# Kernel tuning notes

Measured on AMD Instinct MI355X. Metric: run time of the kernel, lower is better.

Reference implementation:

```python
import jax, jax.numpy as jnp
import numpy as np
import math

# Model config (see init_kwargs)
E = 1024   # emb_size
H = 8      # ffwd_num_head
D = 128    # ffwd_head_size (E == H*D)
NE = 16    # ffwd_num_expert
A = 2      # ffwd_num_expert_active
S = 256    # ffwd_expert_size
B = 2      # batch_size_fwd
T = 2048   # context_window
NUM_BLOCK = 12


def setup_inputs() -> dict:
    key = jax.random.key(0)
    ks = jax.random.split(key, 5)
    x = jax.random.normal(ks[0], (B, T, E), jnp.float32)
    # fc_in_fused: Linear(E, 4E+NE, bias=False), torch weight shape (out,in)
    w_in = 0.02 * jax.random.normal(ks[1], (4 * E + NE, E), jnp.float32)
    # fc_out_fused: Linear(2E, E), std 0.02/sqrt(num_block)
    w_out = (0.02 / math.sqrt(NUM_BLOCK)) * jax.random.normal(ks[2], (E, 2 * E), jnp.float32)
    # k_ffwd/v_ffwd: original (1,H,NE*S,D); stored here as (NE,H,S,D) for per-expert scan
    k_ffwd = 0.02 * jax.random.normal(ks[3], (NE, H, S, D), jnp.float32)
    v_ffwd = 0.02 * jax.random.normal(ks[4], (NE, H, S, D), jnp.float32)
    return {"x": x, "w_in": w_in, "w_out": w_out, "k_ffwd": k_ffwd, "v_ffwd": v_ffwd}


def _rope(t):
    # Standard half-split RoPE, base 10000. t: (B,T,H,D)
    half = t.shape[-1] // 2
    inv_freq = 1.0 / (10000.0 ** (jnp.arange(half, dtype=jnp.float32) / half))
    ang = jnp.arange(t.shape[1], dtype=jnp.float32)[:, None] * inv_freq  # (T, half)
    cos = jnp.cos(ang)[None, :, None, :]
    sin = jnp.sin(ang)[None, :, None, :]
    t1, t2 = t[..., :half], t[..., half:]
    return jnp.concatenate([t1 * cos - t2 * sin, t1 * sin + t2 * cos], axis=-1)


def reference(x, w_in, w_out, k_ffwd, v_ffwd):
    Bx, Tx, _ = x.shape
    h = x @ w_in.T  # (B,T,4E+NE)
    q_f, q_a, k_a, v_a, router_logits = jnp.split(h, [E, 2 * E, 3 * E, 4 * E], axis=-1)

    # top-k routing (order of the k slots is irrelevant: outputs are summed)
    gate_logits, assign = jax.lax.top_k(router_logits, A)  # (B,T,A)
    gate = jax.nn.sigmoid(gate_logits)

    # --- attention half: causal softmax attention, scale 1/sqrt(D), with RoPE ---
    q = _rope(q_a.reshape(Bx, Tx, H, D))
    k = _rope(k_a.reshape(Bx, Tx, H, D))
    v = v_a.reshape(Bx, Tx, H, D)
    scores = jnp.einsum('bqhd,bkhd->bhqk', q, k) / math.sqrt(D)
    causal = jnp.tril(jnp.ones((Tx, Tx), dtype=bool))
    scores = jnp.where(causal, scores, -jnp.inf)
    p = jax.nn.softmax(scores, axis=-1)
    attn_out = jnp.einsum('bhqk,bkhd->bqhd', p, v).reshape(Bx, Tx, E)

    # --- MoE-FFN half, expressed as attention with score_mod log1p(gelu):
    # exp(lse)*softmax recovers sum_s (1+gelu(q.k_s)) v_s; subtracting sum_s v_s
    # leaves sum_s gelu(q.k_s) v_s over the assigned expert's slots. ---
    qf = q_f.reshape(Bx, Tx, H, D)

    def step(acc, ekv):
        e, ke, ve = ekv  # ke, ve: (H,S,D)
        s = jnp.einsum('bthd,hsd->bths', qf, ke)
        a = jax.nn.gelu(s, approximate=False)  # torch F.gelu default = exact erf
        o = jnp.einsum('bths,hsd->bthd', a, ve)
        g = jnp.sum(jnp.where(assign == e, gate, 0.0), axis=-1)  # (B,T)
        return acc + g[..., None, None] * o, None

    acc0 = jnp.zeros((Bx, Tx, H, D), x.dtype)
    ffwd_out, _ = jax.lax.scan(step, acc0, (jnp.arange(NE), k_ffwd, v_ffwd))
    ffwd_out = ffwd_out.reshape(Bx, Tx, E)

    out = jnp.concatenate([attn_out, ffwd_out], axis=-1) @ w_out.T  # (B,T,E)
    return out
```

## Files before the change

kernel.cpp:

```cpp
#include <hip/hip_runtime.h>
#include <hip/hip_bf16.h>
#include <math.h>

#define E 1024
#define NEXP 16
#define HH 8
#define DD 128
#define SS 256
#define BB 2
#define TT 2048
#define BT 4096

typedef __attribute__((ext_vector_type(8))) short bf16x8;
typedef __attribute__((ext_vector_type(4))) float f32x4;

#define GLDS16(g, s) __builtin_amdgcn_global_load_lds( \
    (const __attribute__((address_space(1))) void*)(g), \
    (__attribute__((address_space(3))) void*)(s), 16, 0, 0)

__device__ __forceinline__ ushort f2b(float f) {
    union { float f; unsigned u; } v; v.f = f;
    unsigned r = (v.u + 0x7FFFu + ((v.u >> 16) & 1u)) >> 16;
    return (ushort)r;
}
__device__ __forceinline__ float b2f(ushort u) {
    union { unsigned u; float f; } v; v.u = ((unsigned)u) << 16;
    return v.f;
}
__device__ __forceinline__ float gelu_fast(float x) {
    float u2 = x * x;
    float tu = x * (1.5957691216f + 0.0713548163f * u2);
    float e = __expf(tu);
    float sig = 1.f - __builtin_amdgcn_rcpf(e + 1.f);
    return x * sig;
}

__global__ __launch_bounds__(256) void prep(
    const float* __restrict__ w_in, const float* __restrict__ w_out,
    const float* __restrict__ kf, const float* __restrict__ vf,
    const float* __restrict__ x,
    ushort* __restrict__ wib, ushort* __restrict__ wob,
    ushort* __restrict__ kfb, ushort* __restrict__ vtf,
    float* __restrict__ gval, int* __restrict__ eidx, ushort* __restrict__ xb)
{
    __shared__ float T[64][132];
    const int bx = blockIdx.x;
    const int t = threadIdx.x;

    if (bx >= 3584) {
        const int m = (bx - 3584) * 4 + (t >> 6);
        const int lane = t & 63;

        const float* xp = x + (size_t)m * 1024 + lane * 4;
        float4 xv0 = *(const float4*)(xp);
        float4 xv1 = *(const float4*)(xp + 256);
        float4 xv2 = *(const float4*)(xp + 512);
        float4 xv3 = *(const float4*)(xp + 768);

        {
            const int swrow = (m & 7) << 4;
            char* xrow = (char*)xb + (size_t)m * 2048;
            ushort4 u;
            u.x = f2b(xv0.x); u.y = f2b(xv0.y); u.z = f2b(xv0.z); u.w = f2b(xv0.w);
            *(ushort4*)(xrow + ((lane * 8 + 0 * 512) ^ swrow)) = u;
            u.x = f2b(xv1.x); u.y = f2b(xv1.y); u.z = f2b(xv1.z); u.w = f2b(xv1.w);
            *(ushort4*)(xrow + ((lane * 8 + 1 * 512) ^ swrow)) = u;
            u.x = f2b(xv2.x); u.y = f2b(xv2.y); u.z = f2b(xv2.z); u.w = f2b(xv2.w);
            *(ushort4*)(xrow + ((lane * 8 + 2 * 512) ^ swrow)) = u;
            u.x = f2b(xv3.x); u.y = f2b(xv3.y); u.z = f2b(xv3.z); u.w = f2b(xv3.w);
            *(ushort4*)(xrow + ((lane * 8 + 3 * 512) ^ swrow)) = u;
        }

        float p[16];
        #pragma unroll
        for (int e = 0; e < 16; ++e) {
            const float* wp = w_in + (size_t)(4096 + e) * 1024 + lane * 4;
            float4 w0 = *(const float4*)(wp);
            float4 w1 = *(const float4*)(wp + 256);
            float4 w2 = *(const float4*)(wp + 512);
            float4 w3 = *(const float4*)(wp + 768);
            float s0 = xv0.x * w0.x + xv0.y * w0.y + xv0.z * w0.z + xv0.w * w0.w;
            float s1 = xv1.x * w1.x + xv1.y * w1.y + xv1.z * w1.z + xv1.w * w1.w;
            float s2 = xv2.x * w2.x + xv2.y * w2.y + xv2.z * w2.z + xv2.w * w2.w;
            float s3 = xv3.x * w3.x + xv3.y * w3.y + xv3.z * w3.z + xv3.w * w3.w;
            p[e] = (s0 + s1) + (s2 + s3);
        }
        #pragma unroll
        for (int d = 1; d < 64; d <<= 1) {
            #pragma unroll
            for (int e = 0; e < 16; ++e)
                p[e] += __shfl_xor(p[e], d);
        }
        float best = -1e30f; int bi = 0;
        #pragma unroll
        for (int e = 0; e < 16; ++e)
            if (p[e] > best) { best = p[e]; bi = e; }
        float best2 = -1e30f; int bi2 = 0;
        #pragma unroll
        for (int e = 0; e < 16; ++e)
            if (e != bi && p[e] > best2) { best2 = p[e]; bi2 = e; }

        if (lane == 0) {
            gval[m * 2 + 0] = 1.f / (1.f + __expf(-best));
            gval[m * 2 + 1] = 1.f / (1.f + __expf(-best2));
            eidx[m * 2 + 0] = bi;
            eidx[m * 2 + 1] = bi2;
        }
        return;
    }

    if (bx < 3072) {
        const float* in;
        ushort* outp;
        int kshift, i;
        if (bx < 2048) { in = w_in;  outp = wib; kshift = 10; i = (bx * 256 + t) * 8; }
        else           { in = w_out; outp = wob; kshift = 11; i = ((bx - 2048) * 256 + t) * 8; }
        int row = i >> kshift;
        int colb = (i - (row << kshift)) * 2;
        float4 f0 = *(const float4*)(in + i);
        float4 f1 = *(const float4*)(in + i + 4);
        ushort4 u0, u1;
        u0.x = f2b(f0.x); u0.y = f2b(f0.y); u0.z = f2b(f0.z); u0.w = f2b(f0.w);
        u1.x = f2b(f1.x); u1.y = f2b(f1.y); u1.z = f2b(f1.z); u1.w = f2b(f1.w);
        char* dst = (char*)outp + ((size_t)row << (kshift + 1)) + (colb ^ ((row & 7) << 4));
        *(ushort4*)dst = u0;
        *(ushort4*)(dst + 8) = u1;
        return;
    }

    const int idx = bx - 3072;
    const int st = idx & 3, eh = idx >> 2;
    const int s0 = st * 64;
    const float* kbp = kf + (size_t)eh * SS * DD + (size_t)s0 * DD;
    const float* vbp = vf + (size_t)eh * SS * DD + (size_t)s0 * DD;
    for (int i = t; i < 64 * 32; i += 256) {
        int r = i >> 5, c4 = i & 31;
        float4 f = *(const float4*)(kbp + (size_t)r * DD + c4 * 4);
        ushort4 u;
        u.x = f2b(f.x); u.y = f2b(f.y); u.z = f2b(f.z); u.w = f2b(f.w);
        *(ushort4*)((char*)kfb + ((size_t)eh * 256 + s0 + r) * 256 + ((c4 * 8) ^ ((r & 7) << 4))) = u;
    }
    for (int i = t; i < 64 * 32; i += 256) {
        int r = i >> 5, c4 = i & 31;
        float4 f = *(const float4*)(vbp + (size_t)r * DD + c4 * 4);
        T[r][c4 * 4 + 0] = f.x; T[r][c4 * 4 + 1] = f.y;
        T[r][c4 * 4 + 2] = f.z; T[r][c4 * 4 + 3] = f.w;
    }
    __syncthreads();
    int g = t >> 4, fr = t & 15;
    #pragma unroll
    for (int dd = 0; dd < 8; ++dd) {
        int d = g + dd * 16;
        ushort4 u;
        u.x = f2b(T[4 * fr + 0][d]); u.y = f2b(T[4 * fr + 1][d]);
        u.z = f2b(T[4 * fr + 2][d]); u.w = f2b(T[4 * fr + 3][d]);
        size_t ob = ((size_t)eh * 128 + d) * 512 + s0 * 2;
        *(ushort4*)((char*)vtf + ob + ((8 * fr) ^ ((d & 7) << 4))) = u;
    }
}

template<int BF16OUT>
__global__ __launch_bounds__(256) void gemm_bf16(
    const ushort* __restrict__ A, int lda,
    const ushort* __restrict__ B, int ldb,
    void* __restrict__ Cv, int ldc, int K)
{
    __shared__ ushort As[128 * 64];
    __shared__ ushort Bs[128 * 64];
    const int t = threadIdx.x;
    const int l = t & 63, w = t >> 6;
    const int m0 = blockIdx.y * 128, n0 = blockIdx.x * 128;
    const int wr = w >> 1, wc = w & 1;
    const int fr = l & 15, fg = l >> 4;

    const int srow = w * 32 + (l >> 3);
    const int sboff = (l & 7) * 16;
    const char* Ag = (const char*)A + ((size_t)(m0 + srow) * lda) * 2 + sboff;
    const char* Bg = (const char*)B + ((size_t)(n0 + srow) * ldb) * 2 + sboff;
    const int aswz = (fr & 7) << 4;

    f32x4 acc[4][4];
    #pragma unroll
    for (int i = 0; i < 4; ++i)
        #pragma unroll
        for (int j = 0; j < 4; ++j) { acc[i][j][0]=0.f; acc[i][j][1]=0.f; acc[i][j][2]=0.f; acc[i][j][3]=0.f; }

    for (int k0b = 0; k0b < K * 2; k0b += 128) {
        #pragma unroll
        for (int i = 0; i < 4; ++i) {
            GLDS16(Ag + (size_t)(i * 8) * lda * 2 + k0b, (char*)As + (w * 32 + i * 8) * 128);
            GLDS16(Bg + (size_t)(i * 8) * ldb * 2 + k0b, (char*)Bs + (w * 32 + i * 8) * 128);
        }
        __syncthreads();
        #pragma unroll
        for (int ksub = 0; ksub < 2; ++ksub) {
            bf16x8 a[4], b[4];
            #pragma unroll
            for (int mi = 0; mi < 4; ++mi)
                a[mi] = *(const bf16x8*)((const char*)As + (wr * 64 + mi * 16 + fr) * 128 + ((ksub * 64 + fg * 16) ^ aswz));
            #pragma unroll
            for (int ni = 0; ni < 4; ++ni)
                b[ni] = *(const bf16x8*)((const char*)Bs + (wc * 64 + ni * 16 + fr) * 128 + ((ksub * 64 + fg * 16) ^ aswz));
            #pragma unroll
            for (int mi = 0; mi < 4; ++mi)
                #pragma unroll
                for (int ni = 0; ni < 4; ++ni)
                    acc[mi][ni] = __builtin_amdgcn_mfma_f32_16x16x32_bf16(a[mi], b[ni], acc[mi][ni], 0, 0, 0);
        }
        __syncthreads();
    }
    #pragma unroll
    for (int mi = 0; mi < 4; ++mi)
        #pragma unroll
        for (int ni = 0; ni < 4; ++ni) {
            const int row = m0 + wr * 64 + mi * 16 + fg * 4;
            const int col = n0 + wc * 64 + ni * 16 + fr;
            #pragma unroll
            for (int r = 0; r < 4; ++r) {
                if (BF16OUT)
                    ((ushort*)Cv)[(size_t)(row + r) * ldc + col] = f2b(acc[mi][ni][r]);
                else
                    ((float*)Cv)[(size_t)(row + r) * ldc + col] = acc[mi][ni][r];
            }
        }
}

__global__ __launch_bounds__(256) void gemm1_fused(
    const ushort* __restrict__ A, const ushort* __restrict__ B,
    ushort* __restrict__ hbq,
    ushort* __restrict__ qb, ushort* __restrict__ kb,
    ushort* __restrict__ vtb,
    const int* __restrict__ eidx,
    int* __restrict__ counts, int* __restrict__ plist)
{
    __shared__ ushort sh[128 * 128];
    const int lin = blockIdx.x;
    const int t = threadIdx.x;

    if (lin >= 1024) {
        int* ish = (int*)sh;
        const int e = lin - 1024;
        const int w = t >> 6, lane = t & 63;
        const int base = w * 2048;

        int cnt = 0;
        for (int c = 0; c < 2048; c += 64) {
            bool match = (eidx[base + c + lane] == e);
            unsigned long long mask = __ballot(match);
            cnt += __popcll(mask);
        }
        if (lane == 0) ish[w] = cnt;
        __syncthreads();
        int off = 0;
        #pragma unroll
        for (int i = 0; i < 4; ++i) if (i < w) off += ish[i];
        for (int c = 0; c < 2048; c += 64) {
            bool match = (eidx[base + c + lane] == e);
            unsigned long long mask = __ballot(match);
            int lpre = __popcll(mask & ((1ull << lane) - 1ull));
            if (match) plist[e * BT + off + lpre] = base + c + lane;
            off += __popcll(mask);
        }
        if (t == 0) counts[e] = ish[0] + ish[1] + ish[2] + ish[3];
        return;
    }

    ushort* As = sh;
    ushort* Bs = sh + 128 * 64;
    const int l = t & 63, w = t >> 6;
    const int bxn = lin & 31, by = lin >> 5;
    const int m0 = by * 128, n0 = bxn * 128;
    const int wr = w >> 1, wc = w & 1;
    const int fr = l & 15, fg = l >> 4;

    const int srow = w * 32 + (l >> 3);
    const int sboff = (l & 7) * 16;
    const char* Ag = (const char*)A + ((size_t)(m0 + srow) * 1024) * 2 + sboff;
    const char* Bg = (const char*)B + ((size_t)(n0 + srow) * 1024) * 2 + sboff;
    const int aswz = (fr & 7) << 4;

    f32x4 acc[4][4];
    #pragma unroll
    for (int i = 0; i < 4; ++i)
        #pragma unroll
        for (int j = 0; j < 4; ++j) { acc[i][j][0]=0.f; acc[i][j][1]=0.f; acc[i][j][2]=0.f; acc[i][j][3]=0.f; }

    for (int k0b = 0; k0b < 2048; k0b += 128) {
        #pragma unroll
        for (int i = 0; i < 4; ++i) {
            GLDS16(Ag + (size_t)(i * 8) * 2048 + k0b, (char*)As + (w * 32 + i * 8) * 128);
            GLDS16(Bg + (size_t)(i * 8) * 2048 + k0b, (char*)Bs + (w * 32 + i * 8) * 128);
        }
        __syncthreads();
        #pragma unroll
        for (int ksub = 0; ksub < 2; ++ksub) {
            bf16x8 a[4], b[4];
            #pragma unroll
            for (int mi = 0; mi < 4; ++mi)
                a[mi] = *(const bf16x8*)((const char*)As + (wr * 64 + mi * 16 + fr) * 128 + ((ksub * 64 + fg * 16) ^ aswz));
            #pragma unroll
            for (int ni = 0; ni < 4; ++ni)
                b[ni] = *(const bf16x8*)((const char*)Bs + (wc * 64 + ni * 16 + fr) * 128 + ((ksub * 64 + fg * 16) ^ aswz));
            #pragma unroll
            for (int mi = 0; mi < 4; ++mi)
                #pragma unroll
                for (int ni = 0; ni < 4; ++ni)
                    acc[mi][ni] = __builtin_amdgcn_mfma_f32_16x16x32_bf16(a[mi], b[ni], acc[mi][ni], 0, 0, 0);
        }
        __syncthreads();
    }

    const int region = bxn >> 3;
    const int hd = bxn & 7;

    if (region == 0) {
        #pragma unroll
        for (int mi = 0; mi < 4; ++mi)
            #pragma unroll
            for (int ni = 0; ni < 4; ++ni) {
                const int row = m0 + wr * 64 + mi * 16 + fg * 4;
                const int col = n0 + wc * 64 + ni * 16 + fr;
                #pragma unroll
                for (int r = 0; r < 4; ++r)
                    hbq[(size_t)(row + r) * 1024 + col] = f2b(acc[mi][ni][r]);
            }
    } else if (region == 3) {
        #pragma unroll
        for (int mi = 0; mi < 4; ++mi) {
            const int rowg = m0 + wr * 64 + mi * 16 + fg * 4;
            const int tok = rowg & 2047, bt = rowg >> 11;
            const int bh = bt * 8 + hd;
            #pragma unroll
            for (int ni = 0; ni < 4; ++ni) {
                const int d = wc * 64 + ni * 16 + fr;
                ushort4 u;
                u.x = f2b(acc[mi][ni][0]); u.y = f2b(acc[mi][ni][1]);
                u.z = f2b(acc[mi][ni][2]); u.w = f2b(acc[mi][ni][3]);
                char* dst = (char*)vtb + (size_t)(bh * 128 + d) * 4096
                          + (tok >> 6) * 128 + ((2 * (tok & 63)) ^ ((d & 7) << 4));
                *(ushort4*)dst = u;
            }
        }
    } else {
        #pragma unroll
        for (int mi = 0; mi < 4; ++mi)
            #pragma unroll
            for (int ni = 0; ni < 4; ++ni) {
                const int rl = wr * 64 + mi * 16 + fg * 4;
                const int cl = wc * 64 + ni * 16 + fr;
                #pragma unroll
                for (int r = 0; r < 4; ++r)
                    sh[(rl + r) * 128 + cl] = f2b(acc[mi][ni][r]);
            }
        __syncthreads();
        ushort* outb = (region == 1) ? qb : kb;
        #pragma unroll
        for (int it = 0; it < 4; ++it) {
            const int item = it * 256 + t;
            const int rloc = item >> 3, g = item & 7;
            const int rowg = m0 + rloc;
            const int tok = rowg & 2047, bt = rowg >> 11;
            const int sw = (tok & 7) << 4;
            char* rowbase = (char*)outb + ((size_t)((bt * 8 + hd) * 2048 + tok)) * 256;
            ushort lo[8], hi[8];
            #pragma unroll
            for (int jj = 0; jj < 8; ++jj) {
                const int j = g * 8 + jj;
                float t1 = b2f(sh[rloc * 128 + j]);
                float t2 = b2f(sh[rloc * 128 + 64 + j]);
                float invf = __expf(-(float)j * (9.210340371976184f / 64.f));
                float ang = (float)tok * invf;
                float s, c;
                sincosf(ang, &s, &c);
                lo[jj] = f2b(t1 * c - t2 * s);
                hi[jj] = f2b(t1 * s + t2 * c);
            }
            *(ushort4*)(rowbase + ((16 * g) ^ sw))        = *(ushort4*)&lo[0];
            *(ushort4*)(rowbase + (((16 * g) ^ sw) + 8))  = *(ushort4*)&lo[4];
            *(ushort4*)(rowbase + ((16 * g + 128) ^ sw))       = *(ushort4*)&hi[0];
            *(ushort4*)(rowbase + (((16 * g + 128) ^ sw) + 8)) = *(ushort4*)&hi[4];
        }
    }
}

__global__ __launch_bounds__(512, 1) void attn_mfma(
    const ushort* __restrict__ qb, const ushort* __restrict__ kb,
    const ushort* __restrict__ vtb, ushort* __restrict__ catb)
{
    __shared__ ushort Ks[2][128 * 128];
    __shared__ ushort Vs[2][128 * 128];
    __shared__ ushort Ps[8][16 * 72];
    __shared__ float  LlS[8][16];

    const int t = threadIdx.x, l = t & 63, w = t >> 6;
    const int fr = l & 15, fg = l >> 4;
    const int wl = w & 3, hh = w >> 2;
    const int lin = blockIdx.x;
    const int bh = (lin & 7) * 2 + (lin >> 7);
    const int tpair = (lin >> 3) & 15;
    const int swz = (fr & 7) << 4;
    ushort* Pw = (ushort*)Ps[w];

    #pragma unroll 1
    for (int pass = 0; pass < 2; ++pass) {
        const int qt = pass ? (31 - tpair) : tpair;
        const int qbase = qt * 64;
        const int nkt = (qt + 2) >> 1;
        const int qg = qbase + wl * 16 + fg * 4;

        bf16x8 qreg[4];
        {
            const char* qrow = (const char*)qb + ((size_t)(bh * 2048 + qbase + wl * 16 + fr)) * 256;
            #pragma unroll
            for (int ks = 0; ks < 4; ++ks)
                qreg[ks] = *(const bf16x8*)(qrow + ((ks * 64 + fg * 16) ^ swz));
        }
        {
            const char* ksrc = (const char*)kb + ((size_t)(bh * 2048 + w * 16)) * 256;
            const char* vsrc = (const char*)vtb + ((size_t)(bh * 128 + w * 16)) * 4096;
            #pragma unroll
            for (int i = 0; i < 4; ++i) {
                GLDS16(ksrc + (size_t)(i * 4 + (l >> 4)) * 256 + (l & 15) * 16,
                       (char*)Ks[0] + (w * 16 + i * 4) * 256);
                GLDS16(vsrc + (size_t)(i * 4 + (l >> 4)) * 4096 + (l & 15) * 16,
                       (char*)Vs[0] + (w * 16 + i * 4) * 256);
            }
        }

        f32x4 po[8];
        #pragma unroll
        for (int i = 0; i < 8; ++i) { po[i][0]=0.f; po[i][1]=0.f; po[i][2]=0.f; po[i][3]=0.f; }
        float lrow[4] = {0.f, 0.f, 0.f, 0.f};

        asm volatile("s_waitcnt vmcnt(0)" ::: "memory");
        __syncthreads();

        for (int kt = 0; kt < nkt; ++kt) {
            const int cur = kt & 1;
            if (kt + 1 < nkt) {
                const int kvn = (kt + 1) * 128;
                const char* ksrc = (const char*)kb + ((size_t)(bh * 2048 + kvn + w * 16)) * 256;
                const char* vsrc = (const char*)vtb + ((size_t)(bh * 128 + w * 16)) * 4096 + kvn * 2;
                #pragma unroll
                for (int i = 0; i < 4; ++i) {
                    GLDS16(ksrc + (size_t)(i * 4 + (l >> 4)) * 256 + (l & 15) * 16,
                           (char*)Ks[cur ^ 1] + (w * 16 + i * 4) * 256);
                    GLDS16(vsrc + (size_t)(i * 4 + (l >> 4)) * 4096 + (l & 15) * 16,
                           (char*)Vs[cur ^ 1] + (w * 16 + i * 4) * 256);
                }
            }
            const int kvb = kt * 128;

            f32x4 s[4];
            #pragma unroll
            for (int i = 0; i < 4; ++i) { s[i][0]=0.f; s[i][1]=0.f; s[i][2]=0.f; s[i][3]=0.f; }
            __builtin_amdgcn_s_setprio(1);
            #pragma unroll
            for (int ks = 0; ks < 4; ++ks) {
                #pragma unroll
                for (int fn = 0; fn < 4; ++fn) {
                    const int brow = hh * 64 + fn * 16 + fr;
                    bf16x8 bb = *(const bf16x8*)((const char*)Ks[cur] + brow * 256 + ((ks * 64 + fg * 16) ^ swz));
                    s[fn] = __builtin_amdgcn_mfma_f32_16x16x32_bf16(qreg[ks], bb, s[fn], 0, 0, 0);
                }
            }
            __builtin_amdgcn_s_setprio(0);

            const int colbase = kvb + hh * 64;
            const bool needmask = (colbase + 64 > qbase + wl * 16);
            float ps[4] = {0.f, 0.f, 0.f, 0.f};
            #pragma unroll
            for (int fn = 0; fn < 4; ++fn)
                #pragma unroll
                for (int r = 0; r < 4; ++r) {
                    float v = s[fn][r] * 0.08838834764831845f;
                    bool masked = needmask && (colbase + fn * 16 + fr > qg + r);
                    float p = masked ? 0.f : __expf(v);
                    ps[r] += p;
                    Pw[(fg * 4 + r) * 72 + fn * 16 + fr] = f2b(p);
                }
            #pragma unroll
            for (int r = 0; r < 4; ++r) {
                float s2 = ps[r];
                s2 += __shfl_xor(s2, 1);
                s2 += __shfl_xor(s2, 2);
                s2 += __shfl_xor(s2, 4);
                s2 += __shfl_xor(s2, 8);
                lrow[r] += s2;
            }

            asm volatile("s_waitcnt lgkmcnt(0)" ::: "memory");
            __builtin_amdgcn_sched_barrier(0);

            __builtin_amdgcn_s_setprio(1);
            #pragma unroll
            for (int ks2 = 0; ks2 < 2; ++ks2) {
                bf16x8 pa = *(const bf16x8*)((const char*)Pw + fr * 144 + ks2 * 64 + fg * 16);
                #pragma unroll
                for (int fn2 = 0; fn2 < 8; ++fn2) {
                    const int vrow = fn2 * 16 + fr;
                    bf16x8 bv = *(const bf16x8*)((const char*)Vs[cur] + vrow * 256 + ((hh * 128 + ks2 * 64 + fg * 16) ^ swz));
                    po[fn2] = __builtin_amdgcn_mfma_f32_16x16x32_bf16(pa, bv, po[fn2], 0, 0, 0);
                }
            }
            __builtin_amdgcn_s_setprio(0);

            asm volatile("s_waitcnt vmcnt(0)" ::: "memory");
            __syncthreads();
        }

        if (fr == 0) {
            #pragma unroll
            for (int r = 0; r < 4; ++r)
                LlS[w][fg * 4 + r] = lrow[r];
        }
        __syncthreads();
        float linv[4];
        #pragma unroll
        for (int r = 0; r < 4; ++r)
            linv[r] = 1.f / (lrow[r] + LlS[w ^ 4][fg * 4 + r]);
        float* PO = (float*)&Ks[0][0];
        if (hh == 1) {
            #pragma unroll
            for (int fn2 = 0; fn2 < 8; ++fn2)
                #pragma unroll
                for (int r = 0; r < 4; ++r)
                    PO[(wl * 16 + fg * 4 + r) * 128 + fn2 * 16 + fr] = po[fn2][r];
        }
        __syncthreads();
        if (hh == 0) {
            const int mg = (bh >> 3) * 2048 + qbase + wl * 16 + fg * 4;
            #pragma unroll
            for (int r = 0; r < 4; ++r) {
                const int rswz = ((mg + r) & 7) << 4;
                #pragma unroll
                for (int fn2 = 0; fn2 < 8; ++fn2) {
                    float v = po[fn2][r] + PO[(wl * 16 + fg * 4 + r) * 128 + fn2 * 16 + fr];
                    int colb = ((bh & 7) * 128 + fn2 * 16 + fr) * 2;
                    *(ushort*)((char*)catb + (size_t)(mg + r) * 4096 + (colb ^ rswz)) = f2b(v * linv[r]);
                }
            }
        }
        __syncthreads();
    }
}

__global__ __launch_bounds__(256, 1) void ffn_mfma2(
    const ushort* __restrict__ hbq,
    const float* __restrict__ gv,
    const int* __restrict__ counts,
    const int* __restrict__ plist,
    const ushort* __restrict__ kfb, const ushort* __restrict__ vtf,
    ushort* __restrict__ pairout)
{
    __shared__ ushort Ks[256 * 128];
    __shared__ ushort Vs[128 * 256];
    __shared__ ushort Qs[64 * 128];
    __shared__ ushort Ps[4][16 * 72];

    const int t = threadIdx.x, l = t & 63, w = t >> 6;
    const int fr = l & 15, fg = l >> 4;
    const int half = blockIdx.x, hd = blockIdx.y, e = blockIdx.z;
    const int eh = e * HH + hd;
    const int n_e = counts[e];

    {
        const char* kbase = (const char*)kfb + (size_t)eh * 65536;
        const char* vbase = (const char*)vtf + (size_t)eh * 65536;
        #pragma unroll
        for (int i = 0; i < 16; ++i) {
            GLDS16(kbase + (w * 64 + i * 4) * 256 + l * 16, (char*)Ks + (w * 64 + i * 4) * 256);
            GLDS16(vbase + w * 16384 + i * 1024 + l * 16, (char*)Vs + w * 16384 + i * 1024);
        }
    }
    __syncthreads();

    const int arow = w * 16 + fr;
    const int aswz = (arow & 7) << 4;
    ushort* Pw = (ushort*)Ps[w];
    const int rl4 = l >> 4;
    const int lb = (l & 15) * 16;

    for (int tb = half * 64; tb < n_e; tb += 128) {
        #pragma unroll
        for (int i = 0; i < 4; ++i) {
            int row = w * 16 + i * 4 + rl4;
            int gr = tb + row;
            int p = plist[e * BT + min(gr, n_e - 1)];
            int m = p >> 1;
            const char* src = (const char*)hbq + (size_t)m * 2048 + hd * 256 + (lb ^ ((row & 7) << 4));
            GLDS16(src, (char*)Qs + (w * 16 + i * 4) * 256);
        }
        asm volatile("s_waitcnt vmcnt(0)" ::: "memory");

        f32x4 po[8];
        #pragma unroll
        for (int i = 0; i < 8; ++i) { po[i][0]=0.f; po[i][1]=0.f; po[i][2]=0.f; po[i][3]=0.f; }

        #pragma unroll
        for (int kt = 0; kt < 4; ++kt) {
            const int kvb = kt * 64;
            f32x4 sA[4];
            #pragma unroll
            for (int i = 0; i < 4; ++i) { sA[i][0]=0.f; sA[i][1]=0.f; sA[i][2]=0.f; sA[i][3]=0.f; }
            #pragma unroll
            for (int ks = 0; ks < 4; ++ks) {
                bf16x8 aa = *(const bf16x8*)((const char*)Qs + arow * 256 + ((ks * 64 + fg * 16) ^ aswz));
                #pragma unroll
                for (int fn = 0; fn < 4; ++fn) {
                    const int brow = kvb + fn * 16 + fr;
                    bf16x8 bb = *(const bf16x8*)((const char*)Ks + brow * 256 + ((ks * 64 + fg * 16) ^ ((brow & 7) << 4)));
                    sA[fn] = __builtin_amdgcn_mfma_f32_16x16x32_bf16(aa, bb, sA[fn], 0, 0, 0);
                }
            }
            #pragma unroll
            for (int fn = 0; fn < 4; ++fn)
                #pragma unroll
                for (int r = 0; r < 4; ++r)
                    Pw[(fg * 4 + r) * 72 + fn * 16 + fr] = f2b(gelu_fast(sA[fn][r]));
            asm volatile("s_waitcnt lgkmcnt(0)" ::: "memory");
            #pragma unroll
            for (int ks2 = 0; ks2 < 2; ++ks2) {
                bf16x8 pa = *(const bf16x8*)((const char*)Pw + fr * 144 + ks2 * 64 + fg * 16);
                #pragma unroll
                for (int fn2 = 0; fn2 < 8; ++fn2) {
                    const int vrow = fn2 * 16 + fr;
                    bf16x8 bv = *(const bf16x8*)((const char*)Vs + vrow * 512 + kt * 128 + ((ks2 * 64 + fg * 16) ^ ((vrow & 7) << 4)));
                    po[fn2] = __builtin_amdgcn_mfma_f32_16x16x32_bf16(pa, bv, po[fn2], 0, 0, 0);
                }
            }
        }
        const int rloc = w * 16 + fg * 4;
        #pragma unroll
        for (int r = 0; r < 4; ++r) {
            int gr = tb + rloc + r;
            if (gr < n_e) {
                int p = plist[e * BT + gr];
                float g = gv[p];
                #pragma unroll
                for (int fn2 = 0; fn2 < 8; ++fn2)
                    pairout[(size_t)p * 1024 + hd * DD + fn2 * 16 + fr] = f2b(g * po[fn2][r]);
            }
        }
    }
}

__global__ void combine_kernel(const ushort* __restrict__ po, ushort* __restrict__ catb)
{
    int i = blockIdx.x * blockDim.x + threadIdx.x;
    if (i >= BT * 128) return;
    int m = i >> 7, c = i & 127;
    const ushort* a = po + (size_t)(2 * m) * 1024 + c * 8;
    const ushort* b = po + (size_t)(2 * m + 1) * 1024 + c * 8;
    ushort4 a0 = *(const ushort4*)a, a1 = *(const ushort4*)(a + 4);
    ushort4 b0 = *(const ushort4*)b, b1 = *(const ushort4*)(b + 4);
    ushort4 o0, o1;
    o0.x = f2b(b2f(a0.x) + b2f(b0.x)); o0.y = f2b(b2f(a0.y) + b2f(b0.y));
    o0.z = f2b(b2f(a0.z) + b2f(b0.z)); o0.w = f2b(b2f(a0.w) + b2f(b0.w));
    o1.x = f2b(b2f(a1.x) + b2f(b1.x)); o1.y = f2b(b2f(a1.y) + b2f(b1.y));
    o1.z = f2b(b2f(a1.z) + b2f(b1.z)); o1.w = f2b(b2f(a1.w) + b2f(b1.w));
    char* dst = (char*)catb + (size_t)m * 4096 + 2048 + ((c * 16) ^ ((m & 7) << 4));
    *(ushort4*)dst = o0;
    *(ushort4*)(dst + 8) = o1;
}

extern "C" void kernel_launch(void* const* d_in, const int* in_sizes, int n_in,
                              void* d_out, int out_size, void* d_ws, size_t ws_size,
                              hipStream_t stream)
{
    const float* x     = (const float*)d_in[0];
    const float* w_in  = (const float*)d_in[1];
    const float* w_out = (const float*)d_in[2];
    const float* kf    = (const float*)d_in[3];
    const float* vf    = (const float*)d_in[4];
    float* out = (float*)d_out;

    char* W = (char*)d_ws;
    ushort* hbq     = (ushort*)(W + 0);
    ushort* xb      = (ushort*)(W + 33554432);
    ushort* wib     = (ushort*)(W + 41943040);
    ushort* wob     = (ushort*)(W + 50331648);
    ushort* qb2     = (ushort*)(W + 54525952);
    ushort* kb2     = (ushort*)(W + 62914560);
    ushort* vtb     = (ushort*)(W + 71303168);
    ushort* catb    = (ushort*)(W + 79691776);
    ushort* pairout = (ushort*)(W + 96468992);
    float*  gv      = (float*)(W + 113246208);
    int*    counts  = (int*)(W + 113278976);
    int*    plist   = (int*)(W + 113279040);
    int*    eidx    = (int*)(W + 113541184);
    ushort* kfb     = (ushort*)(W + 113573952);
    ushort* vtf     = (ushort*)(W + 121962560);

    prep<<<4608, 256, 0, stream>>>(w_in, w_out, kf, vf, x,
                                   wib, wob, kfb, vtf, gv, eidx, xb);

    gemm1_fused<<<1040, 256, 0, stream>>>(xb, wib, hbq, qb2, kb2, vtb,
                                          eidx, counts, plist);

    attn_mfma<<<dim3(256), 512, 0, stream>>>(qb2, kb2, vtb, catb);

    ffn_mfma2<<<dim3(2, HH, NEXP), 256, 0, stream>>>(hbq, gv, counts, plist, kfb, vtf, pairout);
    combine_kernel<<<2048, 256, 0, stream>>>(pairout, catb);

    gemm_bf16<0><<<dim3(8, 32), 256, 0, stream>>>(catb, 2048, wob, 2048, out, 1024, 2048);
}
```

Measured before the change: 212.3 us.

## Merge attention and MoE-FFN kernels into one launch with block-index dispatch

The separate causal attention kernel and expert FFN kernel become a single kernel of 512 blocks. The first 256 blocks run attention and the rest run the per-expert FFN, using one shared-memory buffer that is carved up differently for each role. This lets the two independent stages run concurrently on the GPU and removes one launch and the serialization between them. In exchange, FFN blocks now launch 512 threads with half of them idle after the load, and both roles reserve the larger shared-memory footprint, which may limit occupancy.

```diff
diff --git a/kernel.cpp b/kernel.cpp
--- a/kernel.cpp
+++ b/kernel.cpp
@@ -383,169 +383,9 @@
     }
 }
 
-__global__ __launch_bounds__(512, 1) void attn_mfma(
+__global__ __launch_bounds__(512, 1) void attn_ffn(
     const ushort* __restrict__ qb, const ushort* __restrict__ kb,
-    const ushort* __restrict__ vtb, ushort* __restrict__ catb)
-{
-    __shared__ ushort Ks[2][128 * 128];
-    __shared__ ushort Vs[2][128 * 128];
-    __shared__ ushort Ps[8][16 * 72];
-    __shared__ float  LlS[8][16];
-
-    const int t = threadIdx.x, l = t & 63, w = t >> 6;
-    const int fr = l & 15, fg = l >> 4;
-    const int wl = w & 3, hh = w >> 2;
-    const int lin = blockIdx.x;
-    const int bh = (lin & 7) * 2 + (lin >> 7);
-    const int tpair = (lin >> 3) & 15;
-    const int swz = (fr & 7) << 4;
-    ushort* Pw = (ushort*)Ps[w];
-
-    #pragma unroll 1
-    for (int pass = 0; pass < 2; ++pass) {
-        const int qt = pass ? (31 - tpair) : tpair;
-        const int qbase = qt * 64;
-        const int nkt = (qt + 2) >> 1;
-        const int qg = qbase + wl * 16 + fg * 4;
-
-        bf16x8 qreg[4];
-        {
-            const char* qrow = (const char*)qb + ((size_t)(bh * 2048 + qbase + wl * 16 + fr)) * 256;
-            #pragma unroll
-            for (int ks = 0; ks < 4; ++ks)
-                qreg[ks] = *(const bf16x8*)(qrow + ((ks * 64 + fg * 16) ^ swz));
-        }
-        {
-            const char* ksrc = (const char*)kb + ((size_t)(bh * 2048 + w * 16)) * 256;
-            const char* vsrc = (const char*)vtb + ((size_t)(bh * 128 + w * 16)) * 4096;
-            #pragma unroll
-            for (int i = 0; i < 4; ++i) {
-                GLDS16(ksrc + (size_t)(i * 4 + (l >> 4)) * 256 + (l & 15) * 16,
-                       (char*)Ks[0] + (w * 16 + i * 4) * 256);
-                GLDS16(vsrc + (size_t)(i * 4 + (l >> 4)) * 4096 + (l & 15) * 16,
-                       (char*)Vs[0] + (w * 16 + i * 4) * 256);
-            }
-        }
-
-        f32x4 po[8];
-        #pragma unroll
-        for (int i = 0; i < 8; ++i) { po[i][0]=0.f; po[i][1]=0.f; po[i][2]=0.f; po[i][3]=0.f; }
-        float lrow[4] = {0.f, 0.f, 0.f, 0.f};
-
-        asm volatile("s_waitcnt vmcnt(0)" ::: "memory");
-        __syncthreads();
-
-        for (int kt = 0; kt < nkt; ++kt) {
-            const int cur = kt & 1;
-            if (kt + 1 < nkt) {
-                const int kvn = (kt + 1) * 128;
-                const char* ksrc = (const char*)kb + ((size_t)(bh * 2048 + kvn + w * 16)) * 256;
-                const char* vsrc = (const char*)vtb + ((size_t)(bh * 128 + w * 16)) * 4096 + kvn * 2;
-                #pragma unroll
-                for (int i = 0; i < 4; ++i) {
-                    GLDS16(ksrc + (size_t)(i * 4 + (l >> 4)) * 256 + (l & 15) * 16,
-                           (char*)Ks[cur ^ 1] + (w * 16 + i * 4) * 256);
-                    GLDS16(vsrc + (size_t)(i * 4 + (l >> 4)) * 4096 + (l & 15) * 16,
-                           (char*)Vs[cur ^ 1] + (w * 16 + i * 4) * 256);
-                }
-            }
-            const int kvb = kt * 128;
-
-            f32x4 s[4];
-            #pragma unroll
-            for (int i = 0; i < 4; ++i) { s[i][0]=0.f; s[i][1]=0.f; s[i][2]=0.f; s[i][3]=0.f; }
-            __builtin_amdgcn_s_setprio(1);
-            #pragma unroll
-            for (int ks = 0; ks < 4; ++ks) {
-                #pragma unroll
-                for (int fn = 0; fn < 4; ++fn) {
-                    const int brow = hh * 64 + fn * 16 + fr;
-                    bf16x8 bb = *(const bf16x8*)((const char*)Ks[cur] + brow * 256 + ((ks * 64 + fg * 16) ^ swz));
-                    s[fn] = __builtin_amdgcn_mfma_f32_16x16x32_bf16(qreg[ks], bb, s[fn], 0, 0, 0);
-                }
-            }
-            __builtin_amdgcn_s_setprio(0);
-
-            const int colbase = kvb + hh * 64;
-            const bool needmask = (colbase + 64 > qbase + wl * 16);
-            float ps[4] = {0.f, 0.f, 0.f, 0.f};
-            #pragma unroll
-            for (int fn = 0; fn < 4; ++fn)
-                #pragma unroll
-                for (int r = 0; r < 4; ++r) {
-                    float v = s[fn][r] * 0.08838834764831845f;
-                    bool masked = needmask && (colbase + fn * 16 + fr > qg + r);
-                    float p = masked ? 0.f : __expf(v);
-                    ps[r] += p;
-                    Pw[(fg * 4 + r) * 72 + fn * 16 + fr] = f2b(p);
-                }
-            #pragma unroll
-            for (int r = 0; r < 4; ++r) {
-                float s2 = ps[r];
-                s2 += __shfl_xor(s2, 1);
-                s2 += __shfl_xor(s2, 2);
-                s2 += __shfl_xor(s2, 4);
-                s2 += __shfl_xor(s2, 8);
-                lrow[r] += s2;
-            }
-
-            asm volatile("s_waitcnt lgkmcnt(0)" ::: "memory");
-            __builtin_amdgcn_sched_barrier(0);
-
-            __builtin_amdgcn_s_setprio(1);
-            #pragma unroll
-            for (int ks2 = 0; ks2 < 2; ++ks2) {
-                bf16x8 pa = *(const bf16x8*)((const char*)Pw + fr * 144 + ks2 * 64 + fg * 16);
-                #pragma unroll
-                for (int fn2 = 0; fn2 < 8; ++fn2) {
-                    const int vrow = fn2 * 16 + fr;
-                    bf16x8 bv = *(const bf16x8*)((const char*)Vs[cur] + vrow * 256 + ((hh * 128 + ks2 * 64 + fg * 16) ^ swz));
-                    po[fn2] = __builtin_amdgcn_mfma_f32_16x16x32_bf16(pa, bv, po[fn2], 0, 0, 0);
-                }
-            }
-            __builtin_amdgcn_s_setprio(0);
-
-            asm volatile("s_waitcnt vmcnt(0)" ::: "memory");
-            __syncthreads();
-        }
-
-        if (fr == 0) {
-            #pragma unroll
-            for (int r = 0; r < 4; ++r)
-                LlS[w][fg * 4 + r] = lrow[r];
-        }
-        __syncthreads();
-        float linv[4];
-        #pragma unroll
-        for (int r = 0; r < 4; ++r)
-            linv[r] = 1.f / (lrow[r] + LlS[w ^ 4][fg * 4 + r]);
-        float* PO = (float*)&Ks[0][0];
-        if (hh == 1) {
-            #pragma unroll
-            for (int fn2 = 0; fn2 < 8; ++fn2)
-                #pragma unroll
-                for (int r = 0; r < 4; ++r)
-                    PO[(wl * 16 + fg * 4 + r) * 128 + fn2 * 16 + fr] = po[fn2][r];
-        }
-        __syncthreads();
-        if (hh == 0) {
-            const int mg = (bh >> 3) * 2048 + qbase + wl * 16 + fg * 4;
-            #pragma unroll
-            for (int r = 0; r < 4; ++r) {
-                const int rswz = ((mg + r) & 7) << 4;
-                #pragma unroll
-                for (int fn2 = 0; fn2 < 8; ++fn2) {
-                    float v = po[fn2][r] + PO[(wl * 16 + fg * 4 + r) * 128 + fn2 * 16 + fr];
-                    int colb = ((bh & 7) * 128 + fn2 * 16 + fr) * 2;
-                    *(ushort*)((char*)catb + (size_t)(mg + r) * 4096 + (colb ^ rswz)) = f2b(v * linv[r]);
-                }
-            }
-        }
-        __syncthreads();
-    }
-}
-
-__global__ __launch_bounds__(256, 1) void ffn_mfma2(
+    const ushort* __restrict__ vtb, ushort* __restrict__ catb,
     const ushort* __restrict__ hbq,
     const float* __restrict__ gv,
     const int* __restrict__ counts,
@@ -553,93 +393,253 @@
     const ushort* __restrict__ kfb, const ushort* __restrict__ vtf,
     ushort* __restrict__ pairout)
 {
-    __shared__ ushort Ks[256 * 128];
-    __shared__ ushort Vs[128 * 256];
-    __shared__ ushort Qs[64 * 128];
-    __shared__ ushort Ps[4][16 * 72];
-
+    __shared__ __align__(16) char smem[156672];
     const int t = threadIdx.x, l = t & 63, w = t >> 6;
     const int fr = l & 15, fg = l >> 4;
-    const int half = blockIdx.x, hd = blockIdx.y, e = blockIdx.z;
-    const int eh = e * HH + hd;
-    const int n_e = counts[e];
+    const int lin = blockIdx.x;
+
+    if (lin < 256) {
+        ushort* Psb  = (ushort*)(smem + 131072);
+        float*  LlSb = (float*)(smem + 149504);
+
+        const int wl = w & 3, hh = w >> 2;
+        const int bh = (lin & 7) * 2 + (lin >> 7);
+        const int tpair = (lin >> 3) & 15;
+        const int swz = (fr & 7) << 4;
+        ushort* Pw = Psb + w * (16 * 72);
+
+        #pragma unroll 1
+        for (int pass = 0; pass < 2; ++pass) {
+            const int qt = pass ? (31 - tpair) : tpair;
+            const int qbase = qt * 64;
+            const int nkt = (qt + 2) >> 1;
+            const int qg = qbase + wl * 16 + fg * 4;
+
+            bf16x8 qreg[4];
+            {
+                const char* qrow = (const char*)qb + ((size_t)(bh * 2048 + qbase + wl * 16 + fr)) * 256;
+                #pragma unroll
+                for (int ks = 0; ks < 4; ++ks)
+                    qreg[ks] = *(const bf16x8*)(qrow + ((ks * 64 + fg * 16) ^ swz));
+            }
+            {
+                const char* ksrc = (const char*)kb + ((size_t)(bh * 2048 + w * 16)) * 256;
+                const char* vsrc = (const char*)vtb + ((size_t)(bh * 128 + w * 16)) * 4096;
+                #pragma unroll
+                for (int i = 0; i < 4; ++i) {
+                    GLDS16(ksrc + (size_t)(i * 4 + (l >> 4)) * 256 + (l & 15) * 16,
+                           smem + (w * 16 + i * 4) * 256);
+                    GLDS16(vsrc + (size_t)(i * 4 + (l >> 4)) * 4096 + (l & 15) * 16,
+                           smem + 65536 + (w * 16 + i * 4) * 256);
+                }
+            }
+
+            f32x4 po[8];
+            #pragma unroll
+            for (int i = 0; i < 8; ++i) { po[i][0]=0.f; po[i][1]=0.f; po[i][2]=0.f; po[i][3]=0.f; }
+            float lrow[4] = {0.f, 0.f, 0.f, 0.f};
+
+            asm volatile("s_waitcnt vmcnt(0)" ::: "memory");
+            __syncthreads();
+
+            for (int kt = 0; kt < nkt; ++kt) {
+                const int cur = kt & 1;
+                if (kt + 1 < nkt) {
+                    const int kvn = (kt + 1) * 128;
+                    const char* ksrc = (const char*)kb + ((size_t)(bh * 2048 + kvn + w * 16)) * 256;
+                    const char* vsrc = (const char*)vtb + ((size_t)(bh * 128 + w * 16)) * 4096 + kvn * 2;
+                    #pragma unroll
+                    for (int i = 0; i < 4; ++i) {
+                        GLDS16(ksrc + (size_t)(i * 4 + (l >> 4)) * 256 + (l & 15) * 16,
+                               smem + (cur ^ 1) * 32768 + (w * 16 + i * 4) * 256);
+                        GLDS16(vsrc + (size_t)(i * 4 + (l >> 4)) * 4096 + (l & 15) * 16,
+                               smem + 65536 + (cur ^ 1) * 32768 + (w * 16 + i * 4) * 256);
+                    }
+                }
+                const int kvb = kt * 128;
+
+                f32x4 s[4];
+                #pragma unroll
+                for (int i = 0; i < 4; ++i) { s[i][0]=0.f; s[i][1]=0.f; s[i][2]=0.f; s[i][3]=0.f; }
+                __builtin_amdgcn_s_setprio(1);
+                #pragma unroll
+                for (int ks = 0; ks < 4; ++ks) {
+                    #pragma unroll
+                    for (int fn = 0; fn < 4; ++fn) {
+                        const int brow = hh * 64 + fn * 16 + fr;
+                        bf16x8 bb = *(const bf16x8*)(smem + cur * 32768 + brow * 256 + ((ks * 64 + fg * 16) ^ swz));
+                        s[fn] = __builtin_amdgcn_mfma_f32_16x16x32_bf16(qreg[ks], bb, s[fn], 0, 0, 0);
+                    }
+                }
+                __builtin_amdgcn_s_setprio(0);
+
+                const int colbase = kvb + hh * 64;
+                const bool needmask = (colbase + 64 > qbase + wl * 16);
+                float ps[4] = {0.f, 0.f, 0.f, 0.f};
+                #pragma unroll
+                for (int fn = 0; fn < 4; ++fn)
+                    #pragma unroll
+                    for (int r = 0; r < 4; ++r) {
+                        float v = s[fn][r] * 0.08838834764831845f;
+                        bool masked = needmask && (colbase + fn * 16 + fr > qg + r);
+                        float p = masked ? 0.f : __expf(v);
+                        ps[r] += p;
+                        Pw[(fg * 4 + r) * 72 + fn * 16 + fr] = f2b(p);
+                    }
+                #pragma unroll
+                for (int r = 0; r < 4; ++r) {
+                    float s2 = ps[r];
+                    s2 += __shfl_xor(s2, 1);
+                    s2 += __shfl_xor(s2, 2);
+                    s2 += __shfl_xor(s2, 4);
+                    s2 += __shfl_xor(s2, 8);
+                    lrow[r] += s2;
+                }
+
+                asm volatile("s_waitcnt lgkmcnt(0)" ::: "memory");
+                __builtin_amdgcn_sched_barrier(0);
+
+                __builtin_amdgcn_s_setprio(1);
+                #pragma unroll
+                for (int ks2 = 0; ks2 < 2; ++ks2) {
+                    bf16x8 pa = *(const bf16x8*)((const char*)Pw + fr * 144 + ks2 * 64 + fg * 16);
+                    #pragma unroll
+                    for (int fn2 = 0; fn2 < 8; ++fn2) {
+                        const int vrow = fn2 * 16 + fr;
+                        bf16x8 bv = *(const bf16x8*)(smem + 65536 + cur * 32768 + vrow * 256 + ((hh * 128 + ks2 * 64 + fg * 16) ^ swz));
+                        po[fn2] = __builtin_amdgcn_mfma_f32_16x16x32_bf16(pa, bv, po[fn2], 0, 0, 0);
+                    }
+                }
+                __builtin_amdgcn_s_setprio(0);
+
+                asm volatile("s_waitcnt vmcnt(0)" ::: "memory");
+                __syncthreads();
+            }
+
+            if (fr == 0) {
+                #pragma unroll
+                for (int r = 0; r < 4; ++r)
+                    LlSb[w * 16 + fg * 4 + r] = lrow[r];
+            }
+            __syncthreads();
+            float linv[4];
+            #pragma unroll
+            for (int r = 0; r < 4; ++r)
+                linv[r] = 1.f / (lrow[r] + LlSb[(w ^ 4) * 16 + fg * 4 + r]);
+            float* PO = (float*)smem;
+            if (hh == 1) {
+                #pragma unroll
+                for (int fn2 = 0; fn2 < 8; ++fn2)
+                    #pragma unroll
+                    for (int r = 0; r < 4; ++r)
+                        PO[(wl * 16 + fg * 4 + r) * 128 + fn2 * 16 + fr] = po[fn2][r];
+            }
+            __syncthreads();
+            if (hh == 0) {
+                const int mg = (bh >> 3) * 2048 + qbase + wl * 16 + fg * 4;
+                #pragma unroll
+                for (int r = 0; r < 4; ++r) {
+                    const int rswz = ((mg + r) & 7) << 4;
+                    #pragma unroll
+                    for (int fn2 = 0; fn2 < 8; ++fn2) {
+                        float v = po[fn2][r] + PO[(wl * 16 + fg * 4 + r) * 128 + fn2 * 16 + fr];
+                        int colb = ((bh & 7) * 128 + fn2 * 16 + fr) * 2;
+                        *(ushort*)((char*)catb + (size_t)(mg + r) * 4096 + (colb ^ rswz)) = f2b(v * linv[r]);
+                    }
+                }
+            }
+            __syncthreads();
+        }
+        return;
+    }
 
     {
-        const char* kbase = (const char*)kfb + (size_t)eh * 65536;
-        const char* vbase = (const char*)vtf + (size_t)eh * 65536;
-        #pragma unroll
-        for (int i = 0; i < 16; ++i) {
-            GLDS16(kbase + (w * 64 + i * 4) * 256 + l * 16, (char*)Ks + (w * 64 + i * 4) * 256);
-            GLDS16(vbase + w * 16384 + i * 1024 + l * 16, (char*)Vs + w * 16384 + i * 1024);
-        }
-    }
-    __syncthreads();
-
-    const int arow = w * 16 + fr;
-    const int aswz = (arow & 7) << 4;
-    ushort* Pw = (ushort*)Ps[w];
-    const int rl4 = l >> 4;
-    const int lb = (l & 15) * 16;
-
-    for (int tb = half * 64; tb < n_e; tb += 128) {
-        #pragma unroll
-        for (int i = 0; i < 4; ++i) {
-            int row = w * 16 + i * 4 + rl4;
-            int gr = tb + row;
-            int p = plist[e * BT + min(gr, n_e - 1)];
-            int m = p >> 1;
-            const char* src = (const char*)hbq + (size_t)m * 2048 + hd * 256 + (lb ^ ((row & 7) << 4));
-            GLDS16(src, (char*)Qs + (w * 16 + i * 4) * 256);
-        }
-        asm volatile("s_waitcnt vmcnt(0)" ::: "memory");
-
-        f32x4 po[8];
-        #pragma unroll
-        for (int i = 0; i < 8; ++i) { po[i][0]=0.f; po[i][1]=0.f; po[i][2]=0.f; po[i][3]=0.f; }
-
-        #pragma unroll
-        for (int kt = 0; kt < 4; ++kt) {
-            const int kvb = kt * 64;
-            f32x4 sA[4];
-            #pragma unroll
-            for (int i = 0; i < 4; ++i) { sA[i][0]=0.f; sA[i][1]=0.f; sA[i][2]=0.f; sA[i][3]=0.f; }
-            #pragma unroll
-            for (int ks = 0; ks < 4; ++ks) {
-                bf16x8 aa = *(const bf16x8*)((const char*)Qs + arow * 256 + ((ks * 64 + fg * 16) ^ aswz));
-                #pragma unroll
-                for (int fn = 0; fn < 4; ++fn) {
-                    const int brow = kvb + fn * 16 + fr;
-                    bf16x8 bb = *(const bf16x8*)((const char*)Ks + brow * 256 + ((ks * 64 + fg * 16) ^ ((brow & 7) << 4)));
-                    sA[fn] = __builtin_amdgcn_mfma_f32_16x16x32_bf16(aa, bb, sA[fn], 0, 0, 0);
-                }
-            }
-            #pragma unroll
-            for (int fn = 0; fn < 4; ++fn)
-                #pragma unroll
-                for (int r = 0; r < 4; ++r)
-                    Pw[(fg * 4 + r) * 72 + fn * 16 + fr] = f2b(gelu_fast(sA[fn][r]));
-            asm volatile("s_waitcnt lgkmcnt(0)" ::: "memory");
-            #pragma unroll
-            for (int ks2 = 0; ks2 < 2; ++ks2) {
-                bf16x8 pa = *(const bf16x8*)((const char*)Pw + fr * 144 + ks2 * 64 + fg * 16);
-                #pragma unroll
-                for (int fn2 = 0; fn2 < 8; ++fn2) {
-                    const int vrow = fn2 * 16 + fr;
-                    bf16x8 bv = *(const bf16x8*)((const char*)Vs + vrow * 512 + kt * 128 + ((ks2 * 64 + fg * 16) ^ ((vrow & 7) << 4)));
-                    po[fn2] = __builtin_amdgcn_mfma_f32_16x16x32_bf16(pa, bv, po[fn2], 0, 0, 0);
-                }
-            }
-        }
-        const int rloc = w * 16 + fg * 4;
-        #pragma unroll
-        for (int r = 0; r < 4; ++r) {
-            int gr = tb + rloc + r;
-            if (gr < n_e) {
-                int p = plist[e * BT + gr];
-                float g = gv[p];
-                #pragma unroll
-                for (int fn2 = 0; fn2 < 8; ++fn2)
-                    pairout[(size_t)p * 1024 + hd * DD + fn2 * 16 + fr] = f2b(g * po[fn2][r]);
+        ushort* Qs  = (ushort*)(smem + 131072);
+        ushort* Psb = (ushort*)(smem + 147456);
+
+        const int idx = lin - 256;
+        const int half = idx & 1, hd = (idx >> 1) & 7, e = idx >> 4;
+        const int eh = e * HH + hd;
+        const int n_e = counts[e];
+
+        if (w < 4) {
+            const char* kbase = (const char*)kfb + (size_t)eh * 65536;
+            const char* vbase = (const char*)vtf + (size_t)eh * 65536;
+            #pragma unroll
+            for (int i = 0; i < 16; ++i) {
+                GLDS16(kbase + (w * 64 + i * 4) * 256 + l * 16, smem + (w * 64 + i * 4) * 256);
+                GLDS16(vbase + w * 16384 + i * 1024 + l * 16, smem + 65536 + w * 16384 + i * 1024);
+            }
+        }
+        __syncthreads();
+        if (w >= 4) return;
+
+        const int arow = w * 16 + fr;
+        const int aswz = (arow & 7) << 4;
+        ushort* Pw = Psb + w * (16 * 72);
+        const int rl4 = l >> 4;
+        const int lb = (l & 15) * 16;
+
+        for (int tb = half * 64; tb < n_e; tb += 128) {
+            #pragma unroll
+            for (int i = 0; i < 4; ++i) {
+                int row = w * 16 + i * 4 + rl4;
+                int gr = tb + row;
+                int p = plist[e * BT + min(gr, n_e - 1)];
+                int m = p >> 1;
+                const char* src = (const char*)hbq + (size_t)m * 2048 + hd * 256 + (lb ^ ((row & 7) << 4));
+                GLDS16(src, (char*)Qs + (w * 16 + i * 4) * 256);
+            }
+            asm volatile("s_waitcnt vmcnt(0)" ::: "memory");
+
+            f32x4 po[8];
+            #pragma unroll
+            for (int i = 0; i < 8; ++i) { po[i][0]=0.f; po[i][1]=0.f; po[i][2]=0.f; po[i][3]=0.f; }
+
+            #pragma unroll
+            for (int kt = 0; kt < 4; ++kt) {
+                const int kvb = kt * 64;
+                f32x4 sA[4];
+                #pragma unroll
+                for (int i = 0; i < 4; ++i) { sA[i][0]=0.f; sA[i][1]=0.f; sA[i][2]=0.f; sA[i][3]=0.f; }
+                #pragma unroll
+                for (int ks = 0; ks < 4; ++ks) {
+                    bf16x8 aa = *(const bf16x8*)((const char*)Qs + arow * 256 + ((ks * 64 + fg * 16) ^ aswz));
+                    #pragma unroll
+                    for (int fn = 0; fn < 4; ++fn) {
+                        const int brow = kvb + fn * 16 + fr;
+                        bf16x8 bb = *(const bf16x8*)(smem + brow * 256 + ((ks * 64 + fg * 16) ^ ((brow & 7) << 4)));
+                        sA[fn] = __builtin_amdgcn_mfma_f32_16x16x32_bf16(aa, bb, sA[fn], 0, 0, 0);
+                    }
+                }
+                #pragma unroll
+                for (int fn = 0; fn < 4; ++fn)
+                    #pragma unroll
+                    for (int r = 0; r < 4; ++r)
+                        Pw[(fg * 4 + r) * 72 + fn * 16 + fr] = f2b(gelu_fast(sA[fn][r]));
+                asm volatile("s_waitcnt lgkmcnt(0)" ::: "memory");
+                #pragma unroll
+                for (int ks2 = 0; ks2 < 2; ++ks2) {
+                    bf16x8 pa = *(const bf16x8*)((const char*)Pw + fr * 144 + ks2 * 64 + fg * 16);
+                    #pragma unroll
+                    for (int fn2 = 0; fn2 < 8; ++fn2) {
+                        const int vrow = fn2 * 16 + fr;
+                        bf16x8 bv = *(const bf16x8*)(smem + 65536 + vrow * 512 + kt * 128 + ((ks2 * 64 + fg * 16) ^ ((vrow & 7) << 4)));
+                        po[fn2] = __builtin_amdgcn_mfma_f32_16x16x32_bf16(pa, bv, po[fn2], 0, 0, 0);
+                    }
+                }
+            }
+            const int rloc = w * 16 + fg * 4;
+            #pragma unroll
+            for (int r = 0; r < 4; ++r) {
+                int gr = tb + rloc + r;
+                if (gr < n_e) {
+                    int p = plist[e * BT + gr];
+                    float g = gv[p];
+                    #pragma unroll
+                    for (int fn2 = 0; fn2 < 8; ++fn2)
+                        pairout[(size_t)p * 1024 + hd * DD + fn2 * 16 + fr] = f2b(g * po[fn2][r]);
+                }
             }
         }
     }
@@ -698,9 +698,9 @@
     gemm1_fused<<<1040, 256, 0, stream>>>(xb, wib, hbq, qb2, kb2, vtb,
                                           eidx, counts, plist);
 
-    attn_mfma<<<dim3(256), 512, 0, stream>>>(qb2, kb2, vtb, catb);
-
-    ffn_mfma2<<<dim3(2, HH, NEXP), 256, 0, stream>>>(hbq, gv, counts, plist, kfb, vtf, pairout);
+    attn_ffn<<<512, 512, 0, stream>>>(qb2, kb2, vtb, catb,
+                                      hbq, gv, counts, plist, kfb, vtf, pairout);
+
     combine_kernel<<<2048, 256, 0, stream>>>(pairout, catb);
 
     gemm_bf16<0><<<dim3(8, 32), 256, 0, stream>>>(catb, 2048, wob, 2048, out, 1024, 2048);
```

Result: no change. 209.7 us (-1.3%).
